# Kernel tuning notes

Measured on AMD Instinct MI355X. Metric: run time of the kernel, lower is better.

Reference implementation:

```python
import jax, jax.numpy as jnp
import numpy as np

N_F = 100000   # station (feature) nodes
N_H = 49152    # healpix nodes (12*4^6)
E = 400000     # edges per timestep
T_IN = 12
T_OUT = 12
H = 64         # hidden_size (must equal 64: cat with Linear(1,64) output)
A_H = 2 * H    # AttentionReadout hidden_size


def setup_inputs() -> dict:
    key = jax.random.key(0)
    ks = jax.random.split(key, 20)
    feat = jax.random.normal(ks[0], (N_F, T_IN, 1), dtype=jnp.float32)
    enc_src = jax.random.randint(ks[1], (E,), 0, N_F, dtype=jnp.int32)
    enc_dst = jax.random.randint(ks[2], (E,), 0, N_H, dtype=jnp.int32)
    dec_src = jax.random.randint(ks[3], (E,), 0, N_H, dtype=jnp.int32)
    dec_dst = jax.random.randint(ks[4], (E,), 0, N_F, dtype=jnp.int32)
    s = 0.05
    return {
        'feat': feat,
        'enc_src': enc_src, 'enc_dst': enc_dst,
        'dec_src': dec_src, 'dec_dst': dec_dst,
        # per-timestep encoder GraphConv(1 -> H) weights
        'W_enc': jax.random.normal(ks[5], (T_IN, 1, H), jnp.float32) * s,
        'b_enc': jnp.zeros((T_IN, H), jnp.float32),
        # MLP processor over time: Linear(T_IN -> T_OUT) + ReLU
        'W_proc': jax.random.normal(ks[6], (T_IN, T_OUT), jnp.float32) * s,
        'b_proc': jnp.zeros((T_OUT,), jnp.float32),
        # per-timestep decoder GraphConv(H -> H)
        'W_dec': jax.random.normal(ks[7], (T_OUT, H, H), jnp.float32) * s,
        'b_dec': jnp.zeros((T_OUT, H), jnp.float32),
        # decoder self.linears = Linear(1, 64)
        'W_lin': jax.random.normal(ks[8], (1, H), jnp.float32) * s,
        'b_lin': jnp.zeros((H,), jnp.float32),
        # AttentionReadout: score MLP (H -> 2H -> 1), output proj (H -> 1)
        'W_a1': jax.random.normal(ks[9], (H, A_H), jnp.float32) * s,
        'b_a1': jnp.zeros((A_H,), jnp.float32),
        'W_a2': jax.random.normal(ks[10], (A_H, 1), jnp.float32) * s,
        'b_a2': jnp.zeros((1,), jnp.float32),
        'W_o': jax.random.normal(ks[11], (H, 1), jnp.float32) * s,
        'b_o': jnp.zeros((1,), jnp.float32),
    }


def _gcn_norms(src, dst, n_src, n_dst):
    # DGL GraphConv norm='both': deg clamped to min 1, ^-0.5
    ones = jnp.ones(src.shape[0], jnp.float32)
    out_deg = jnp.maximum(jax.ops.segment_sum(ones, src, num_segments=n_src), 1.0)
    in_deg = jnp.maximum(jax.ops.segment_sum(ones, dst, num_segments=n_dst), 1.0)
    return out_deg ** -0.5, in_deg ** -0.5


def reference(feat, enc_src, enc_dst, dec_src, dec_dst,
              W_enc, b_enc, W_proc, b_proc, W_dec, b_dec,
              W_lin, b_lin, W_a1, b_a1, W_a2, b_a2, W_o, b_o):
    c_se, c_de = _gcn_norms(enc_src, enc_dst, N_F, N_H)
    c_sd, c_dd = _gcn_norms(dec_src, dec_dst, N_H, N_F)

    # ---- Graph_Encoder: per-t GraphConv(station -> healpix), 1 -> H ----
    x = jnp.nan_to_num(feat)                                  # [N_f, T_in, 1]
    msg = x * c_se[:, None, None]
    agg = jax.ops.segment_sum(msg[enc_src], enc_dst, num_segments=N_H)  # [N_h, T_in, 1]
    h_enc = jax.nn.leaky_relu(
        jnp.einsum('nti,tih->nth', agg * c_de[:, None, None], W_enc) + b_enc)  # [N_h, T_in, H]

    # ---- MLP_Processor: Linear over the time axis, T_in -> T_out, ReLU ----
    h_proc = jax.nn.relu(jnp.einsum('nth,to->noh', h_enc, W_proc)
                         + b_proc[:, None])                    # [N_h, T_out, H]
    h_proc_t = jnp.swapaxes(h_proc, 0, 1)                      # [T_out, N_h, H]

    # ---- Graph_Decoder: per-t GraphConv(healpix -> station) + Linear(prev) + AttentionReadout ----
    def step(y_prev, inp):
        h_t, W_t, b_t = inp                                    # h_t: [N_h, H]
        m = h_t * c_sd[:, None]
        a = jax.ops.segment_sum(m[dec_src], dec_dst, num_segments=N_F)  # [N_f, H]
        space1 = jax.nn.leaky_relu((a * c_dd[:, None]) @ W_t + b_t)     # [N_f, H]
        space2 = y_prev @ W_lin + b_lin                                 # [N_f, H]
        stacked = jnp.stack([space1, space2], axis=0)                   # [2, N_f, H]
        scores = jnp.tanh(stacked @ W_a1 + b_a1) @ W_a2 + b_a2          # [2, N_f, 1]
        alpha = jax.nn.softmax(scores, axis=0)
        states = jnp.sum(alpha * stacked, axis=0)                       # [N_f, H]
        y = states @ W_o + b_o                                          # [N_f, 1]
        return y, y

    y0 = x[:, -1]                                              # t{input_length-1}
    _, ys = jax.lax.scan(step, y0, (h_proc_t, W_dec, b_dec))
    return ys                                                  # [T_out, N_f, 1]
```

## Files before the change

kernel.cpp:

```cpp
#include <hip/hip_runtime.h>
#include <hip/hip_bf16.h>
#include <hip/hip_fp16.h>

#define NF 100000
#define NH 49152
#define EDG 400000
#define SLOTD 24
#define SLOTE 32

typedef __attribute__((ext_vector_type(8))) short short8;
typedef __attribute__((ext_vector_type(4))) float float4v;
typedef unsigned short u16;
typedef unsigned int u32;

__device__ __forceinline__ u16 f2b(float x) {
    u32 u = __float_as_uint(x);
    u32 r = u + 0x7FFFu + ((u >> 16) & 1u);
    return (u16)(r >> 16);
}
__device__ __forceinline__ u32 cvt_pk(float lo, float hi) {
    u32 r;
    asm("v_cvt_pk_bf16_f32 %0, %1, %2" : "=v"(r) : "v"(lo), "v"(hi));
    return r;
}
__device__ __forceinline__ __half2 h2(u32 v) { union { u32 u; __half2 h; } c; c.u = v; return c.h; }
__device__ __forceinline__ float fast_tanh(float x) {
    float t = __builtin_amdgcn_exp2f(x * 2.885390081777927f);
    return fmaf(-2.0f, __builtin_amdgcn_rcpf(t + 1.0f), 1.0f);
}

#define PN1 (NF * 12)
#define PN2 (NH * SLOTE)
#define PN3 298304
#define PN4 384
#define PREB 12000
__global__ void init_all(u32* __restrict__ csrD32, u32* __restrict__ csrE,
                         u32* __restrict__ degcnt, u32* __restrict__ mzero, int zstride,
                         const float* __restrict__ W_dec, const float* __restrict__ W_a1,
                         u16* __restrict__ fragWdec, u16* __restrict__ fragWa1,
                         const float* __restrict__ W_lin, const float* __restrict__ b_lin,
                         const float* __restrict__ b_a1, const float* __restrict__ W_o,
                         float* __restrict__ uvs, const float* __restrict__ W_a2,
                         float* __restrict__ gtab) {
    __shared__ float uvl[256];
    const int b = blockIdx.x;
    if (b < PREB) {
        int i = b * 256 + threadIdx.x;
        if (i < PN1) csrD32[i] = ((u32)NH << 16) | (u32)NH;
        else if (i < PN1 + PN2) csrE[i - PN1] = 0u;
        else if (i < PN1 + PN2 + PN3) degcnt[i - PN1 - PN2] = 0u;
        else if (i < PN1 + PN2 + PN3 + PN4) {
            int j = i - PN1 - PN2 - PN3;
            mzero[(j >> 7) * (size_t)zstride + (j & 127)] = 0u;
        }
    } else if (b < PREB + 28) {
        int gid = (b - PREB) * 256 + threadIdx.x;
        if (gid >= 7168) return;
        int L = gid & 63;
        int f = gid >> 6;
        int q = L >> 4, cb = L & 15;
        if (f < 96) {
            int fr = f & 7;
            int c = fr >> 1, kc = fr & 1;
            int k0 = kc * 32 + q * 8;
            int nn = c * 16 + cb;
            int t = f >> 3;
            #pragma unroll
            for (int j = 0; j < 8; ++j)
                fragWdec[(f * 64 + L) * 8 + j] = f2b(W_dec[t * 4096 + (k0 + j) * 64 + nn]);
        } else {
            int fr = f - 96;
            int c2 = fr >> 1, kc = fr & 1;
            int k0 = kc * 32 + q * 8;
            int nn = c2 * 16 + cb;
            #pragma unroll
            for (int j = 0; j < 8; ++j)
                fragWa1[(fr * 64 + L) * 8 + j] = f2b(W_a1[(k0 + j) * 128 + nn]);
        }
    } else if (b == PREB + 28) {
        int k = threadIdx.x;
        if (k < 128) {
            float su = 0.f, sv = 0.f;
            for (int h = 0; h < 64; ++h) {
                su = fmaf(W_lin[h], W_a1[h * 128 + k], su);
                sv = fmaf(b_lin[h], W_a1[h * 128 + k], sv);
            }
            uvs[k] = su;
            uvs[128 + k] = sv + b_a1[k];
            if (k == 0) {
                float a = 0.f, bb = 0.f;
                for (int h = 0; h < 64; ++h) {
                    a = fmaf(W_lin[h], W_o[h], a);
                    bb = fmaf(b_lin[h], W_o[h], bb);
                }
                uvs[256] = a;
                uvs[257] = bb;
            }
        }
    } else {
        int k = threadIdx.x;
        if (k < 128) {
            float su = 0.f, sv = 0.f;
            for (int h = 0; h < 64; ++h) {
                su = fmaf(W_lin[h], W_a1[h * 128 + k], su);
                sv = fmaf(b_lin[h], W_a1[h * 128 + k], sv);
            }
            uvl[k] = su;
            uvl[128 + k] = sv + b_a1[k];
        }
        __syncthreads();
        int i = (b - PREB - 29) * 256 + threadIdx.x;
        if (i <= 16384) {
            float y = fmaf((float)i, 1.f / 256.f, -32.f);
            float s = 0.f;
            for (int kk = 0; kk < 128; ++kk)
                s = fmaf(fast_tanh(fmaf(y, uvl[kk], uvl[128 + kk])), W_a2[kk], s);
            gtab[i] = s;
        }
    }
}

__global__ void fill_slotted(const int* __restrict__ enc_src, const int* __restrict__ enc_dst,
                             const int* __restrict__ dec_src, const int* __restrict__ dec_dst,
                             int* __restrict__ cntD, u16* __restrict__ csrD, float* __restrict__ deg_sd,
                             int* __restrict__ cntE, u32* __restrict__ csrE, float* __restrict__ deg_se) {
    int e = blockIdx.x * 256 + threadIdx.x;
    if (e >= EDG) return;
    int ds = dec_src[e], dd = dec_dst[e];
    int i1 = atomicAdd(&cntD[dd], 1);
    if (i1 < SLOTD) csrD[(size_t)dd * SLOTD + i1] = (u16)ds;
    atomicAdd(&deg_sd[ds], 1.0f);
    int es = enc_src[e], ed = enc_dst[e];
    int i2 = atomicAdd(&cntE[ed], 1);
    if (i2 < SLOTE) csrE[(size_t)ed * SLOTE + i2] = (u32)es;
    atomicAdd(&deg_se[es], 1.0f);
}

__global__ __launch_bounds__(256) void enc_make(
    const float* __restrict__ feat, const float* __restrict__ deg_se,
    const int* __restrict__ cntE, const u32* __restrict__ csrE,
    const float* __restrict__ deg_sd, const float* __restrict__ W_enc,
    const float* __restrict__ b_enc, const float* __restrict__ W_proc,
    const float* __restrict__ b_proc, u16* __restrict__ m, size_t cstride) {
    __shared__ __align__(16) float aggl[4][12];
    const int tid = threadIdx.x, lane = tid & 63, wid = tid >> 6;
    const int n = blockIdx.x * 4 + wid;
    const int q = lane >> 2, l = lane & 3;
    int cntRaw = cntE[n];
    int cnt = cntRaw > SLOTE ? SLOTE : cntRaw;
    const u32* cp = csrE + (size_t)n * SLOTE;
    float4 a = {0.f, 0.f, 0.f, 0.f};
    if (l < 3) {
        for (int e = q; e < cnt; e += 16) {
            u32 s = cp[e];
            float c = rsqrtf(fmaxf(deg_se[s], 1.0f));
            float4 w = *(const float4*)(feat + (size_t)s * 12 + l * 4);
            w.x = (w.x != w.x) ? 0.f : w.x; w.y = (w.y != w.y) ? 0.f : w.y;
            w.z = (w.z != w.z) ? 0.f : w.z; w.w = (w.w != w.w) ? 0.f : w.w;
            a.x = fmaf(w.x, c, a.x); a.y = fmaf(w.y, c, a.y);
            a.z = fmaf(w.z, c, a.z); a.w = fmaf(w.w, c, a.w);
        }
    }
    #pragma unroll
    for (int mm = 4; mm < 64; mm <<= 1) {
        a.x += __shfl_xor(a.x, mm); a.y += __shfl_xor(a.y, mm);
        a.z += __shfl_xor(a.z, mm); a.w += __shfl_xor(a.w, mm);
    }
    if (q == 0 && l < 3) *(float4*)(&aggl[wid][l * 4]) = a;
    asm volatile("s_waitcnt lgkmcnt(0)" ::: "memory");

    const int h = lane;
    float cde = rsqrtf(fmaxf((float)cntRaw, 1.0f));
    float csd = rsqrtf(fmaxf(deg_sd[n], 1.0f));
    float he[12];
    #pragma unroll
    for (int ti = 0; ti < 12; ++ti) {
        float av = aggl[wid][ti] * cde;
        float x = fmaf(av, W_enc[ti * 64 + h], b_enc[ti * 64 + h]);
        he[ti] = x > 0.f ? x : 0.01f * x;
    }
    #pragma unroll
    for (int c = 0; c < 3; ++c) {
        float s0v[4];
        #pragma unroll
        for (int tt = 0; tt < 4; ++tt) {
            int t = c * 4 + tt;
            float s = b_proc[t];
            #pragma unroll
            for (int ti = 0; ti < 12; ++ti) s = fmaf(he[ti], W_proc[ti * 12 + t], s);
            s0v[tt] = fmaxf(s, 0.f) * csd;
        }
        u16 r0 = __half_as_ushort(__float2half(s0v[0]));
        u16 r1 = __half_as_ushort(__float2half(s0v[1]));
        u16 r2 = __half_as_ushort(__float2half(s0v[2]));
        u16 r3 = __half_as_ushort(__float2half(s0v[3]));
        u32 o0 = ((u32)r1 << 16) | r0;
        u32 o1 = ((u32)r3 << 16) | r2;
        u32* dst = (u32*)(m + c * cstride + (size_t)n * 256 + h * 4);
        dst[0] = o0; dst[1] = o1;
    }
}

__global__ __launch_bounds__(256) void enc_gather(const float* __restrict__ feat,
                                                  const float* __restrict__ deg_se,
                                                  const int* __restrict__ cntE,
                                                  const u32* __restrict__ csrE,
                                                  float* __restrict__ agg) {
    const int tid = threadIdx.x, lane = tid & 63, wid = tid >> 6;
    const int grp = lane >> 2, l = lane & 3;
    const int dst = blockIdx.x * 64 + wid * 16 + grp;
    int cnt = cntE[dst];
    if (cnt > SLOTE) cnt = SLOTE;
    const u32* cp = csrE + (size_t)dst * SLOTE;
    float4 a = {0.f, 0.f, 0.f, 0.f};
    if (l < 3) {
        for (int e = 0; e < cnt; ++e) {
            u32 s = cp[e];
            float c = rsqrtf(fmaxf(deg_se[s], 1.0f));
            float4 w = *(const float4*)(feat + (size_t)s * 12 + l * 4);
            w.x = (w.x != w.x) ? 0.f : w.x; w.y = (w.y != w.y) ? 0.f : w.y;
            w.z = (w.z != w.z) ? 0.f : w.z; w.w = (w.w != w.w) ? 0.f : w.w;
            a.x = fmaf(w.x, c, a.x); a.y = fmaf(w.y, c, a.y);
            a.z = fmaf(w.z, c, a.z); a.w = fmaf(w.w, c, a.w);
        }
    }
    *(float4*)(agg + (size_t)dst * 16 + l * 4) = a;
}

__global__ void make_chunk(const float* __restrict__ agg, const int* __restrict__ cntE,
                           const float* __restrict__ deg_sd, const float* __restrict__ W_enc,
                           const float* __restrict__ b_enc, const float* __restrict__ W_proc,
                           const float* __restrict__ b_proc, u16* __restrict__ m, int t0) {
    int gid = blockIdx.x * 256 + threadIdx.x;
    if (gid >= NH * 64) return;
    int n = gid >> 6, h = gid & 63;
    float cde = rsqrtf(fmaxf((float)cntE[n], 1.0f));
    float csd = rsqrtf(fmaxf(deg_sd[n], 1.0f));
    float he[12];
    #pragma unroll
    for (int ti = 0; ti < 12; ++ti) {
        float a = agg[n * 16 + ti] * cde;
        float x = fmaf(a, W_enc[ti * 64 + h], b_enc[ti * 64 + h]);
        he[ti] = x > 0.f ? x : 0.01f * x;
    }
    u16 r[4];
    #pragma unroll
    for (int tt = 0; tt < 4; ++tt) {
        int t = t0 + tt;
        float s = b_proc[t];
        #pragma unroll
        for (int ti = 0; ti < 12; ++ti) s = fmaf(he[ti], W_proc[ti * 12 + t], s);
        s = fmaxf(s, 0.f) * csd;
        r[tt] = __half_as_ushort(__float2half(s));
    }
    u32 o0 = ((u32)r[1] << 16) | r[0];
    u32 o1 = ((u32)r[3] << 16) | r[2];
    u32* dst = (u32*)(m + (size_t)n * 256 + h * 4);
    dst[0] = o0; dst[1] = o1;
}

__device__ __forceinline__ void acc4(__half2* a8, const u16* mrow, u32 lo, u32 hi) {
    int s0 = (int)(lo & 0xFFFF), s1 = (int)(lo >> 16);
    int s2 = (int)(hi & 0xFFFF), s3 = (int)(hi >> 16);
    const uint4* r0 = (const uint4*)(mrow + (size_t)s0 * 256);
    const uint4* r1 = (const uint4*)(mrow + (size_t)s1 * 256);
    const uint4* r2 = (const uint4*)(mrow + (size_t)s2 * 256);
    const uint4* r3 = (const uint4*)(mrow + (size_t)s3 * 256);
    uint4 A0 = r0[0], B0 = r0[1];
    uint4 A1 = r1[0], B1 = r1[1];
    uint4 A2 = r2[0], B2 = r2[1];
    uint4 A3 = r3[0], B3 = r3[1];
    a8[0] = __hadd2(a8[0], __hadd2(__hadd2(h2(A0.x), h2(A1.x)), __hadd2(h2(A2.x), h2(A3.x))));
    a8[1] = __hadd2(a8[1], __hadd2(__hadd2(h2(A0.y), h2(A1.y)), __hadd2(h2(A2.y), h2(A3.y))));
    a8[2] = __hadd2(a8[2], __hadd2(__hadd2(h2(A0.z), h2(A1.z)), __hadd2(h2(A2.z), h2(A3.z))));
    a8[3] = __hadd2(a8[3], __hadd2(__hadd2(h2(A0.w), h2(A1.w)), __hadd2(h2(A2.w), h2(A3.w))));
    a8[4] = __hadd2(a8[4], __hadd2(__hadd2(h2(B0.x), h2(B1.x)), __hadd2(h2(B2.x), h2(B3.x))));
    a8[5] = __hadd2(a8[5], __hadd2(__hadd2(h2(B0.y), h2(B1.y)), __hadd2(h2(B2.y), h2(B3.y))));
    a8[6] = __hadd2(a8[6], __hadd2(__hadd2(h2(B0.z), h2(B1.z)), __hadd2(h2(B2.z), h2(B3.z))));
    a8[7] = __hadd2(a8[7], __hadd2(__hadd2(h2(B0.w), h2(B1.w)), __hadd2(h2(B2.w), h2(B3.w))));
}

__global__ __launch_bounds__(256, 4) void dec_batch(
    const u16* __restrict__ mbase, const int* __restrict__ cntD, const u16* __restrict__ csrD,
    const u16* __restrict__ fragWdec, const u16* __restrict__ fragWa1,
    const float* __restrict__ b_dec, const float* __restrict__ b_a1,
    const float* __restrict__ W_a2, const float* __restrict__ W_o,
    float* __restrict__ S1, float* __restrict__ PW, int t0p, size_t mstride) {
    __shared__ __align__(16) u16 zs[18432];

    const u16* m = mbase + (size_t)blockIdx.y * mstride;
    const int t0 = t0p + blockIdx.y * 4;
    const int tid = threadIdx.x, lane = tid & 63, wid = tid >> 6;
    const int nw = blockIdx.x * 64 + wid * 16;
    const int g16 = lane >> 4, c16 = lane & 15;
    u16* zw0 = zs + wid * 4608;

    int cdw[4]; float cdd[4]; int nnv[4];
    uint4 qa[4];
    #pragma unroll
    for (int k = 0; k < 4; ++k) {
        int n = nw + g16 * 4 + k;
        bool v = (n < NF);
        nnv[k] = v ? n : 0;
        int cd = cntD[nnv[k]];
        cdd[k] = v ? rsqrtf(fmaxf((float)cd, 1.0f)) : 0.f;
        cdw[k] = v ? (cd > SLOTD ? SLOTD : cd) : 0;
        qa[k] = *(const uint4*)(csrD + (size_t)nnv[k] * SLOTD);
    }
    int cdmax = max(max(cdw[0], cdw[1]), max(cdw[2], cdw[3]));

    __half2 acc[4][8];
    #pragma unroll
    for (int k = 0; k < 4; ++k)
        #pragma unroll
        for (int i = 0; i < 8; ++i)
            acc[k][i] = __half2{__half(0.f), __half(0.f)};

    const u16* mrow = m + c16 * 16;
    #pragma unroll
    for (int k = 0; k < 4; ++k) if (cdw[k] > 0) acc4(acc[k], mrow, qa[k].x, qa[k].y);
    #pragma unroll
    for (int k = 0; k < 4; ++k) if (cdw[k] > 4) acc4(acc[k], mrow, qa[k].z, qa[k].w);
    if (__any(cdmax > 8)) {
        #pragma unroll
        for (int k = 0; k < 4; ++k) if (cdw[k] > 8) qa[k] = *(const uint4*)(csrD + (size_t)nnv[k] * SLOTD + 8);
        #pragma unroll
        for (int k = 0; k < 4; ++k) if (cdw[k] > 8) acc4(acc[k], mrow, qa[k].x, qa[k].y);
        #pragma unroll
        for (int k = 0; k < 4; ++k) if (cdw[k] > 12) acc4(acc[k], mrow, qa[k].z, qa[k].w);
        if (__any(cdmax > 16)) {
            #pragma unroll
            for (int k = 0; k < 4; ++k) if (cdw[k] > 16) qa[k] = *(const uint4*)(csrD + (size_t)nnv[k] * SLOTD + 16);
            #pragma unroll
            for (int k = 0; k < 4; ++k) if (cdw[k] > 16) acc4(acc[k], mrow, qa[k].x, qa[k].y);
            #pragma unroll
            for (int k = 0; k < 4; ++k) if (cdw[k] > 20) acc4(acc[k], mrow, qa[k].z, qa[k].w);
        }
    }

    #pragma unroll
    for (int k = 0; k < 4; ++k) {
        int j = g16 * 4 + k;
        float s = cdd[k];
        #pragma unroll
        for (int p = 0; p < 2; ++p) {
            float2 c0 = __half22float2(acc[k][0 * 2 + p]);
            float2 c1 = __half22float2(acc[k][1 * 2 + p]);
            float2 c2 = __half22float2(acc[k][2 * 2 + p]);
            float2 c3 = __half22float2(acc[k][3 * 2 + p]);
            u32 oA0 = cvt_pk(c0.x * s, c1.x * s);
            u32 oA1 = cvt_pk(c2.x * s, c3.x * s);
            u32 oB0 = cvt_pk(c0.y * s, c1.y * s);
            u32 oB1 = cvt_pk(c2.y * s, c3.y * s);
            u32* dA = (u32*)(zw0 + (2 * p) * 1152 + j * 72 + c16 * 4);
            u32* dB = (u32*)(zw0 + (2 * p + 1) * 1152 + j * 72 + c16 * 4);
            dA[0] = oA0; dA[1] = oA1;
            dB[0] = oB0; dB[1] = oB1;
        }
    }
    asm volatile("s_waitcnt lgkmcnt(0)" ::: "memory");

    for (int tt = 0; tt < 4; ++tt) {
        const int t = t0 + tt;
        u16* zw = zw0 + tt * 1152;
        const u16* ab = zw + c16 * 72 + g16 * 8;
        short8 a0 = *(const short8*)ab;
        short8 a1 = *(const short8*)(ab + 32);

        const u16* fw = fragWdec + (size_t)t * 4096;
        float4v C1[4];
        #pragma unroll
        for (int cc = 0; cc < 4; ++cc) {
            float4v z4 = {0.f, 0.f, 0.f, 0.f};
            short8 b0 = *(const short8*)(fw + (cc * 2 + 0) * 512 + lane * 8);
            short8 b1 = *(const short8*)(fw + (cc * 2 + 1) * 512 + lane * 8);
            z4 = __builtin_amdgcn_mfma_f32_16x16x32_bf16(a0, b0, z4, 0, 0, 0);
            C1[cc] = __builtin_amdgcn_mfma_f32_16x16x32_bf16(a1, b1, z4, 0, 0, 0);
        }

        float pw[4] = {0.f, 0.f, 0.f, 0.f};
        #pragma unroll
        for (int cc = 0; cc < 4; ++cc) {
            float bt = b_dec[t * 64 + cc * 16 + c16];
            float wo = W_o[cc * 16 + c16];
            #pragma unroll
            for (int r = 0; r < 4; ++r) {
                float xx = C1[cc][r] + bt;
                float sp = xx > 0.f ? xx : 0.01f * xx;
                pw[r] = fmaf(sp, wo, pw[r]);
                zw[(g16 * 4 + r) * 72 + cc * 16 + c16] = f2b(sp);
            }
        }
        asm volatile("s_waitcnt lgkmcnt(0)" ::: "memory");
        short8 sa0 = *(const short8*)ab;
        short8 sa1 = *(const short8*)(ab + 32);

        float p1[4] = {0.f, 0.f, 0.f, 0.f};
        #pragma unroll
        for (int half = 0; half < 2; ++half) {
            float4v C2[4];
            #pragma unroll
            for (int cc = 0; cc < 4; ++cc) {
                int c8 = half * 4 + cc;
                float4v z4 = {0.f, 0.f, 0.f, 0.f};
                short8 b0 = *(const short8*)(fragWa1 + (c8 * 2 + 0) * 512 + lane * 8);
                short8 b1 = *(const short8*)(fragWa1 + (c8 * 2 + 1) * 512 + lane * 8);
                z4 = __builtin_amdgcn_mfma_f32_16x16x32_bf16(sa0, b0, z4, 0, 0, 0);
                C2[cc] = __builtin_amdgcn_mfma_f32_16x16x32_bf16(sa1, b1, z4, 0, 0, 0);
            }
            #pragma unroll
            for (int cc = 0; cc < 4; ++cc) {
                int k = (half * 4 + cc) * 16 + c16;
                float ba = b_a1[k], wa = W_a2[k];
                #pragma unroll
                for (int r = 0; r < 4; ++r)
                    p1[r] = fmaf(fast_tanh(C2[cc][r] + ba), wa, p1[r]);
            }
        }

        #pragma unroll
        for (int mm = 1; mm < 16; mm <<= 1) {
            #pragma unroll
            for (int r = 0; r < 4; ++r) {
                p1[r] += __shfl_xor(p1[r], mm);
                pw[r] += __shfl_xor(pw[r], mm);
            }
        }

        if (c16 == 0) {
            #pragma unroll
            for (int r = 0; r < 4; ++r) {
                int n = nw + g16 * 4 + r;
                if (n < NF) {
                    S1[(size_t)t * NF + n] = p1[r];
                    PW[(size_t)t * NF + n] = pw[r];
                }
            }
        }
    }
}

__global__ __launch_bounds__(256) void dec_scan(
    const float* __restrict__ S1, const float* __restrict__ PW,
    const float* __restrict__ gtab, const float* __restrict__ uvs,
    const float* __restrict__ feat, const float* __restrict__ b_a2p,
    const float* __restrict__ b_op, float* __restrict__ out) {
    const int n = blockIdx.x * 256 + threadIdx.x;
    if (n >= NF) return;
    float s1v[12], pwv[12];
    #pragma unroll
    for (int t = 0; t < 12; ++t) {
        s1v[t] = S1[(size_t)t * NF + n];
        pwv[t] = PW[(size_t)t * NF + n];
    }
    const float wlo = uvs[256], blo = uvs[257], ba2 = b_a2p[0], bo = b_op[0];
    float yp = feat[n * 12 + 11];
    yp = (yp != yp) ? 0.f : yp;
    #pragma unroll
    for (int t = 0; t < 12; ++t) {
        float xf = fminf(fmaxf(fmaf(yp, 256.f, 8192.f), 0.f), 16383.f);
        int idx = (int)xf;
        float fr = xf - (float)idx;
        float g0 = gtab[idx], g1 = gtab[idx + 1];
        float p2 = fmaf(g1 - g0, fr, g0);
        float s1s = s1v[t] + ba2, s2s = p2 + ba2;
        float mx = fmaxf(s1s, s2s);
        float e1 = __expf(s1s - mx), e2 = __expf(s2s - mx);
        float y = (e1 * pwv[t] + e2 * fmaf(wlo, yp, blo)) / (e1 + e2) + bo;
        out[(size_t)t * NF + n] = y;
        yp = y;
    }
}

extern "C" void kernel_launch(void* const* d_in, const int* in_sizes, int n_in,
                              void* d_out, int out_size, void* d_ws, size_t ws_size,
                              hipStream_t stream) {
    const float* feat   = (const float*)d_in[0];
    const int* enc_src  = (const int*)d_in[1];
    const int* enc_dst  = (const int*)d_in[2];
    const int* dec_src  = (const int*)d_in[3];
    const int* dec_dst  = (const int*)d_in[4];
    const float* W_enc  = (const float*)d_in[5];
    const float* b_enc  = (const float*)d_in[6];
    const float* W_proc = (const float*)d_in[7];
    const float* b_proc = (const float*)d_in[8];
    const float* W_dec  = (const float*)d_in[9];
    const float* b_dec  = (const float*)d_in[10];
    const float* W_lin  = (const float*)d_in[11];
    const float* b_lin  = (const float*)d_in[12];
    const float* W_a1   = (const float*)d_in[13];
    const float* b_a1   = (const float*)d_in[14];
    const float* W_a2   = (const float*)d_in[15];
    const float* b_a2   = (const float*)d_in[16];
    const float* W_o    = (const float*)d_in[17];
    const float* b_o    = (const float*)d_in[18];
    float* out = (float*)d_out;

    float* W = (float*)d_ws;
    float* deg_se   = W;
    float* deg_sd   = W + 100000;
    int*   cntD     = (int*)(W + 149152);
    int*   cntE     = (int*)(W + 249152);
    float* uvs      = W + 298304;
    u16*   fragWdec = (u16*)(W + 298624);
    u16*   fragWa1  = (u16*)(W + 323200);
    float* agg      = W + 327296;
    float* S1       = W + 1113728;
    float* PW       = W + 2313728;
    u16*   csrD     = (u16*)(W + 3513728);
    u32*   csrE     = (u32*)(W + 4713728);
    float* gtab     = W + 6286592;
    u16*   m_ws     = (u16*)(W + 6303104);

    const size_t CSTRIDE = (size_t)(NH + 1) * 256;
    const size_t need_full = ((size_t)6303104 + 3 * CSTRIDE / 2) * 4;
    const bool full = ws_size >= need_full;
    const int zstride = full ? (int)(CSTRIDE / 2) : 0;

    init_all<<<PREB + 29 + 65, 256, 0, stream>>>((u32*)csrD, csrE, (u32*)W,
                                                 (u32*)m_ws + (size_t)NH * 128, zstride,
                                                 W_dec, W_a1, fragWdec, fragWa1,
                                                 W_lin, b_lin, b_a1, W_o, uvs, W_a2, gtab);
    fill_slotted<<<(EDG + 255) / 256, 256, 0, stream>>>(enc_src, enc_dst, dec_src, dec_dst,
                                                        cntD, csrD, deg_sd, cntE, csrE, deg_se);

    const int dec_grid = (NF + 63) / 64;
    if (full) {
        enc_make<<<NH / 4, 256, 0, stream>>>(feat, deg_se, cntE, csrE, deg_sd,
                                             W_enc, b_enc, W_proc, b_proc, m_ws, CSTRIDE);
        dec_batch<<<dim3(dec_grid, 3), 256, 0, stream>>>(m_ws, cntD, csrD, fragWdec, fragWa1,
                                                         b_dec, b_a1, W_a2, W_o, S1, PW,
                                                         0, CSTRIDE);
    } else {
        enc_gather<<<NH / 64, 256, 0, stream>>>(feat, deg_se, cntE, csrE, agg);
        for (int c = 0; c < 3; ++c) {
            make_chunk<<<(NH * 64) / 256, 256, 0, stream>>>(agg, cntE, deg_sd, W_enc, b_enc,
                                                            W_proc, b_proc, m_ws, 4 * c);
            dec_batch<<<dim3(dec_grid, 1), 256, 0, stream>>>(m_ws, cntD, csrD, fragWdec, fragWa1,
                                                             b_dec, b_a1, W_a2, W_o, S1, PW,
                                                             4 * c, 0);
        }
    }
    dec_scan<<<(NF + 255) / 256, 256, 0, stream>>>(S1, PW, gtab, uvs, feat, b_a2, b_o, out);
}
```

Baseline: 350.4 us.

## Drop csrE zero-fill, hoist readout weights to registers, split decoder launch per chunk

Stops zero-initialising the encoder slotted CSR array in init_all and shrinks that kernel's grid to match. Loads b_a1, W_a2 and W_o into registers once per thread instead of reloading them inside the timestep loop. Replaces the single 3-chunk dec_batch launch with three sequential launches over offset m_ws pointers, which may improve cache locality per chunk but adds launch overhead and loses concurrency. Dropping the csrE clear assumes unused slots are never read, which relies on the slot counts.

```diff
diff --git a/kernel.cpp b/kernel.cpp
--- a/kernel.cpp
+++ b/kernel.cpp
@@ -30,11 +30,10 @@
 }
 
 #define PN1 (NF * 12)
-#define PN2 (NH * SLOTE)
 #define PN3 298304
 #define PN4 384
-#define PREB 12000
-__global__ void init_all(u32* __restrict__ csrD32, u32* __restrict__ csrE,
+#define PREB 5856
+__global__ void init_all(u32* __restrict__ csrD32,
                          u32* __restrict__ degcnt, u32* __restrict__ mzero, int zstride,
                          const float* __restrict__ W_dec, const float* __restrict__ W_a1,
                          u16* __restrict__ fragWdec, u16* __restrict__ fragWa1,
@@ -47,10 +46,9 @@
     if (b < PREB) {
         int i = b * 256 + threadIdx.x;
         if (i < PN1) csrD32[i] = ((u32)NH << 16) | (u32)NH;
-        else if (i < PN1 + PN2) csrE[i - PN1] = 0u;
-        else if (i < PN1 + PN2 + PN3) degcnt[i - PN1 - PN2] = 0u;
-        else if (i < PN1 + PN2 + PN3 + PN4) {
-            int j = i - PN1 - PN2 - PN3;
+        else if (i < PN1 + PN3) degcnt[i - PN1] = 0u;
+        else if (i < PN1 + PN3 + PN4) {
+            int j = i - PN1 - PN3;
             mzero[(j >> 7) * (size_t)zstride + (j & 127)] = 0u;
         }
     } else if (b < PREB + 28) {
@@ -360,6 +358,16 @@
     }
     asm volatile("s_waitcnt lgkmcnt(0)" ::: "memory");
 
+    float baw[8], waw[8], wov[4];
+    #pragma unroll
+    for (int c8 = 0; c8 < 8; ++c8) {
+        int k = c8 * 16 + c16;
+        baw[c8] = b_a1[k];
+        waw[c8] = W_a2[k];
+    }
+    #pragma unroll
+    for (int cc = 0; cc < 4; ++cc) wov[cc] = W_o[cc * 16 + c16];
+
     for (int tt = 0; tt < 4; ++tt) {
         const int t = t0 + tt;
         u16* zw = zw0 + tt * 1152;
@@ -382,7 +390,7 @@
         #pragma unroll
         for (int cc = 0; cc < 4; ++cc) {
             float bt = b_dec[t * 64 + cc * 16 + c16];
-            float wo = W_o[cc * 16 + c16];
+            float wo = wov[cc];
             #pragma unroll
             for (int r = 0; r < 4; ++r) {
                 float xx = C1[cc][r] + bt;
@@ -410,8 +418,8 @@
             }
             #pragma unroll
             for (int cc = 0; cc < 4; ++cc) {
-                int k = (half * 4 + cc) * 16 + c16;
-                float ba = b_a1[k], wa = W_a2[k];
+                int c8 = half * 4 + cc;
+                float ba = baw[c8], wa = waw[c8];
                 #pragma unroll
                 for (int r = 0; r < 4; ++r)
                     p1[r] = fmaf(fast_tanh(C2[cc][r] + ba), wa, p1[r]);
@@ -517,7 +525,7 @@
     const bool full = ws_size >= need_full;
     const int zstride = full ? (int)(CSTRIDE / 2) : 0;
 
-    init_all<<<PREB + 29 + 65, 256, 0, stream>>>((u32*)csrD, csrE, (u32*)W,
+    init_all<<<PREB + 29 + 65, 256, 0, stream>>>((u32*)csrD, (u32*)W,
                                                  (u32*)m_ws + (size_t)NH * 128, zstride,
                                                  W_dec, W_a1, fragWdec, fragWa1,
                                                  W_lin, b_lin, b_a1, W_o, uvs, W_a2, gtab);
@@ -528,9 +536,12 @@
     if (full) {
         enc_make<<<NH / 4, 256, 0, stream>>>(feat, deg_se, cntE, csrE, deg_sd,
                                              W_enc, b_enc, W_proc, b_proc, m_ws, CSTRIDE);
-        dec_batch<<<dim3(dec_grid, 3), 256, 0, stream>>>(m_ws, cntD, csrD, fragWdec, fragWa1,
-                                                         b_dec, b_a1, W_a2, W_o, S1, PW,
-                                                         0, CSTRIDE);
+        for (int c = 0; c < 3; ++c) {
+            dec_batch<<<dim3(dec_grid, 1), 256, 0, stream>>>(m_ws + (size_t)c * CSTRIDE,
+                                                             cntD, csrD, fragWdec, fragWa1,
+                                                             b_dec, b_a1, W_a2, W_o, S1, PW,
+                                                             4 * c, 0);
+        }
     } else {
         enc_gather<<<NH / 64, 256, 0, stream>>>(feat, deg_se, cntE, csrE, agg);
         for (int c = 0; c < 3; ++c) {
```

Result: slower. 381.4 us (+8.9%).
